# Optimization experiments

Measured on AMD Instinct MI355X. Metric: run time of the kernel, lower is better.

Reference implementation:

```python
import jax, jax.numpy as jnp
import numpy as np

N_PAPER = 200000
N_MESH = 30000
N = N_PAPER + N_MESH
D_PAPER = 512
D_MESH = 128
E_TRAIN = 2000000
E_POS = 500000
E_NEG = 500000


def setup_inputs() -> dict:
    key = jax.random.key(0)
    ks = jax.random.split(key, 32)

    def w(k, shape, fan_in):
        return jax.random.normal(k, shape, jnp.float32) / np.float32(np.sqrt(fan_in))

    inp = {}
    inp['x_paper'] = jax.random.normal(ks[0], (N_PAPER, D_PAPER), jnp.float32)
    inp['x_mesh'] = jax.random.normal(ks[1], (N_MESH, D_MESH), jnp.float32)
    # input transforms (stored as [in, out]; y = x @ W + b)
    inp['tp_w'] = w(ks[2], (D_PAPER, 16), D_PAPER)
    inp['tp_b'] = jnp.zeros((16,), jnp.float32)
    inp['tm_w'] = w(ks[3], (D_MESH, 16), D_MESH)
    inp['tm_b'] = jnp.zeros((16,), jnp.float32)
    # RGCN layers: basis decomposition W_r = sum_b comp[r,b] * basis[b]
    inp['comp1'] = w(ks[4], (2, 4), 4)
    inp['basis1'] = w(ks[5], (4, 16, 32), 16)
    inp['root1'] = w(ks[6], (16, 32), 16)
    inp['bias1'] = jnp.zeros((32,), jnp.float32)
    inp['comp2'] = w(ks[7], (2, 4), 4)
    inp['basis2'] = w(ks[8], (4, 32, 32), 32)
    inp['root2'] = w(ks[9], (32, 32), 32)
    inp['bias2'] = jnp.zeros((32,), jnp.float32)
    inp['comp3'] = w(ks[10], (2, 4), 4)
    inp['basis3'] = w(ks[11], (4, 32, 16), 32)
    inp['root3'] = w(ks[12], (32, 16), 32)
    inp['bias3'] = jnp.zeros((16,), jnp.float32)
    # decode linears (16 -> 16)
    inp['dpp_w'] = w(ks[13], (16, 16), 16)
    inp['dpp_b'] = jnp.zeros((16,), jnp.float32)
    inp['dpm_w'] = w(ks[14], (16, 16), 16)
    inp['dpm_b'] = jnp.zeros((16,), jnp.float32)
    # graph structure
    inp['train_edge_index'] = jax.random.randint(ks[15], (2, E_TRAIN), 0, N, jnp.int64)
    inp['train_edge_type'] = jax.random.randint(ks[16], (E_TRAIN,), 0, 2, jnp.int64)
    inp['pos_edge_index'] = jax.random.randint(ks[17], (2, E_POS), 0, N, jnp.int64)
    inp['pos_edge_type'] = jnp.sort(jax.random.randint(ks[18], (E_POS,), 0, 2, jnp.int64))
    inp['neg_edge_index'] = jax.random.randint(ks[19], (2, E_NEG), 0, N, jnp.int64)
    inp['neg_edge_type'] = jnp.sort(jax.random.randint(ks[20], (E_NEG,), 0, 2, jnp.int64))
    return inp


def rgcn(x, src, dst, etype, comp, basis, root, bias):
    # W: [R, in, out] from basis decomposition
    W = jnp.einsum('rb,bio->rio', comp, basis)
    # relation-typed message per edge (R == 2: compute both, select)
    xs = x[src]                                   # [E, in]  gather
    m = jnp.where((etype == 0)[:, None], xs @ W[0], xs @ W[1])  # [E, out]
    n = x.shape[0]
    agg = jax.ops.segment_sum(m, dst, num_segments=n)           # scatter-add
    deg = jax.ops.segment_sum(jnp.ones((src.shape[0],), x.dtype), dst, num_segments=n)
    agg = agg / jnp.maximum(deg, 1.0)[:, None]                   # mean aggregation
    return agg + x @ root + bias


def reference(x_paper, x_mesh, tp_w, tp_b, tm_w, tm_b,
              comp1, basis1, root1, bias1,
              comp2, basis2, root2, bias2,
              comp3, basis3, root3, bias3,
              dpp_w, dpp_b, dpm_w, dpm_b,
              train_edge_index, train_edge_type,
              pos_edge_index, pos_edge_type,
              neg_edge_index, neg_edge_type):
    # encode
    x = jnp.concatenate([x_paper @ tp_w + tp_b, x_mesh @ tm_w + tm_b], axis=0)
    src, dst = train_edge_index[0], train_edge_index[1]
    x = jax.nn.relu(rgcn(x, src, dst, train_edge_type, comp1, basis1, root1, bias1))
    x = jax.nn.relu(rgcn(x, src, dst, train_edge_type, comp2, basis2, root2, bias2))
    z = rgcn(x, src, dst, train_edge_type, comp3, basis3, root3, bias3)

    # decode: edge types are sorted, so per-edge type-select equals the
    # original mask-then-concat ordering [type0 ..., type1 ...]
    def edge_scores(ei, et):
        zs, zd = z[ei[0]], z[ei[1]]
        p = jnp.where((et == 0)[:, None], zs @ dpp_w + dpp_b, zs @ dpm_w + dpm_b)
        return (p * zd).sum(-1)

    return jnp.concatenate([edge_scores(pos_edge_index, pos_edge_type),
                            edge_scores(neg_edge_index, neg_edge_type)], axis=0)
```

## Files before the change

### kernel.cpp

```cpp
#include <hip/hip_runtime.h>

#define NPAPER 200000
#define NMESH  30000
#define NNODES 230000
#define ETRAIN 2000000
#define EPOS   500000
#define ENEG   500000

__device__ __forceinline__ void fma4(float4& a, float s, const float4 w) {
    a.x = fmaf(s, w.x, a.x);
    a.y = fmaf(s, w.y, a.y);
    a.z = fmaf(s, w.z, a.z);
    a.w = fmaf(s, w.w, a.w);
}

template <int D>
__global__ __launch_bounds__(256) void encode_kernel(
    const float* __restrict__ x, const float* __restrict__ w,
    const float* __restrict__ bias, float* __restrict__ out, int nrows) {
    __shared__ float wlds[D * 20];
    __shared__ float blds[16];
    for (int i = threadIdx.x; i < D * 16; i += 256)
        wlds[(i >> 4) * 20 + (i & 15)] = w[i];
    if (threadIdx.x < 16) blds[threadIdx.x] = bias[threadIdx.x];
    __syncthreads();

    const int lane = threadIdx.x & 63;
    const int row = blockIdx.x * 4 + (threadIdx.x >> 6);
    if (row >= nrows) return;

    const float* xr = x + (size_t)row * D;
    float4 acc[4];
#pragma unroll
    for (int g = 0; g < 4; g++) acc[g] = make_float4(0.f, 0.f, 0.f, 0.f);

#pragma unroll
    for (int t = 0; t < D / 64; t++) {
        const float xv = xr[t * 64 + lane];
        const float* wr = wlds + (t * 64 + lane) * 20;
#pragma unroll
        for (int g = 0; g < 4; g++)
            fma4(acc[g], xv, *reinterpret_cast<const float4*>(wr + 4 * g));
    }

#pragma unroll
    for (int g = 0; g < 4; g++) {
#pragma unroll
        for (int off = 32; off; off >>= 1) {
            acc[g].x += __shfl_xor(acc[g].x, off);
            acc[g].y += __shfl_xor(acc[g].y, off);
            acc[g].z += __shfl_xor(acc[g].z, off);
            acc[g].w += __shfl_xor(acc[g].w, off);
        }
    }
    if (lane == 0) {
        float4* orow = reinterpret_cast<float4*>(out + (size_t)row * 16);
#pragma unroll
        for (int g = 0; g < 4; g++) {
            const float4 b4 = *reinterpret_cast<const float4*>(blds + 4 * g);
            float4 o;
            o.x = acc[g].x + b4.x;
            o.y = acc[g].y + b4.y;
            o.z = acc[g].z + b4.z;
            o.w = acc[g].w + b4.w;
            orow[g] = o;
        }
    }
}

__global__ __launch_bounds__(256) void hist_kernel(const int* __restrict__ dst,
                                                   int* __restrict__ cnt) {
    const int e = blockIdx.x * 256 + threadIdx.x;
    if (e >= ETRAIN) return;
    atomicAdd(cnt + dst[e], 1);
}

__global__ __launch_bounds__(256) void scan1_kernel(const int* __restrict__ in,
                                                    int* __restrict__ out,
                                                    int* __restrict__ bsum,
                                                    int n) {
    __shared__ int s[256];
    const int tid = threadIdx.x;
    const int i = blockIdx.x * 256 + tid;
    const int v = (i < n) ? in[i] : 0;
    s[tid] = v;
    __syncthreads();
#pragma unroll
    for (int off = 1; off < 256; off <<= 1) {
        const int t = (tid >= off) ? s[tid - off] : 0;
        __syncthreads();
        s[tid] += t;
        __syncthreads();
    }
    if (i < n) out[i] = s[tid] - v;
    if (tid == 255) bsum[blockIdx.x] = s[255];
}

__global__ __launch_bounds__(256) void scan2_kernel(int* __restrict__ bsum,
                                                    int nb) {
    __shared__ int s[256];
    const int tid = threadIdx.x;
    int carry = 0;
    for (int base = 0; base < nb; base += 256) {
        const int i = base + tid;
        const int v = (i < nb) ? bsum[i] : 0;
        s[tid] = v;
        __syncthreads();
#pragma unroll
        for (int off = 1; off < 256; off <<= 1) {
            const int t = (tid >= off) ? s[tid - off] : 0;
            __syncthreads();
            s[tid] += t;
            __syncthreads();
        }
        if (i < nb) bsum[i] = s[tid] - v + carry;
        const int tot = s[255];
        __syncthreads();
        carry += tot;
    }
}

__global__ __launch_bounds__(256) void scan3_kernel(int* __restrict__ out,
                                                    const int* __restrict__ bsum,
                                                    int n) {
    const int i = blockIdx.x * 256 + threadIdx.x;
    if (i < n) out[i] += bsum[blockIdx.x];
}

__global__ __launch_bounds__(256) void fill_kernel(
    const int* __restrict__ src, const int* __restrict__ dst,
    const int* __restrict__ et, const int* __restrict__ rowptr,
    int* __restrict__ fc, int* __restrict__ esorted) {
    const int e = blockIdx.x * 256 + threadIdx.x;
    if (e >= ETRAIN) return;
    const int d = dst[e];
    const int pos = rowptr[d] + atomicAdd(fc + d, 1);
    esorted[pos] = src[e] | (et[e] << 24);
}

template <int IN, int OUT, bool RELU>
__global__ __launch_bounds__(256) void rgcn_gather_kernel(
    const float* __restrict__ x, const int* __restrict__ rowptr,
    const int* __restrict__ cnt, const int* __restrict__ esorted,
    const float* __restrict__ comp, const float* __restrict__ basis,
    const float* __restrict__ root, const float* __restrict__ bias,
    float* __restrict__ out) {
    constexpr int QP = OUT / 4;
    __shared__ float wlds[2 * IN * OUT];
    __shared__ float rlds[IN * OUT];
    __shared__ float blds[OUT];
    for (int i = threadIdx.x; i < 2 * IN * OUT; i += 256) {
        const int r = i / (IN * OUT);
        const int rem = i - r * IN * OUT;
        float v = 0.f;
#pragma unroll
        for (int b = 0; b < 4; b++)
            v = fmaf(comp[r * 4 + b], basis[b * IN * OUT + rem], v);
        wlds[i] = v;
    }
    for (int i = threadIdx.x; i < IN * OUT; i += 256) rlds[i] = root[i];
    if (threadIdx.x < OUT) blds[threadIdx.x] = bias[threadIdx.x];
    __syncthreads();

    const int gtid = blockIdx.x * 256 + threadIdx.x;
    const int n = gtid / QP;
    const int g = gtid % QP;
    if (n >= NNODES) return;

    const int begin = rowptr[n];
    const int c = cnt[n];

    float4 acc = make_float4(0.f, 0.f, 0.f, 0.f);
    for (int i = 0; i < c; i++) {
        const int pk = esorted[begin + i];
        const int s = pk & 0x00FFFFFF;
        const float* Wt = wlds + (pk >> 24) * (IN * OUT);
        const float4* xs = reinterpret_cast<const float4*>(x + (size_t)s * IN);
#pragma unroll
        for (int q = 0; q < IN / 4; q++) {
            const float4 xv = xs[q];
            const float* wq = Wt + (q * 4) * OUT + 4 * g;
            fma4(acc, xv.x, *reinterpret_cast<const float4*>(wq));
            fma4(acc, xv.y, *reinterpret_cast<const float4*>(wq + OUT));
            fma4(acc, xv.z, *reinterpret_cast<const float4*>(wq + 2 * OUT));
            fma4(acc, xv.w, *reinterpret_cast<const float4*>(wq + 3 * OUT));
        }
    }
    const float inv = 1.0f / fmaxf((float)c, 1.0f);
    float4 o = *reinterpret_cast<const float4*>(blds + 4 * g);
    o.x = fmaf(acc.x, inv, o.x);
    o.y = fmaf(acc.y, inv, o.y);
    o.z = fmaf(acc.z, inv, o.z);
    o.w = fmaf(acc.w, inv, o.w);

    const float4* xn = reinterpret_cast<const float4*>(x + (size_t)n * IN);
#pragma unroll
    for (int q = 0; q < IN / 4; q++) {
        const float4 xv = xn[q];
        const float* rq = rlds + (q * 4) * OUT + 4 * g;
        fma4(o, xv.x, *reinterpret_cast<const float4*>(rq));
        fma4(o, xv.y, *reinterpret_cast<const float4*>(rq + OUT));
        fma4(o, xv.z, *reinterpret_cast<const float4*>(rq + 2 * OUT));
        fma4(o, xv.w, *reinterpret_cast<const float4*>(rq + 3 * OUT));
    }
    if (RELU) {
        o.x = fmaxf(o.x, 0.f);
        o.y = fmaxf(o.y, 0.f);
        o.z = fmaxf(o.z, 0.f);
        o.w = fmaxf(o.w, 0.f);
    }
    reinterpret_cast<float4*>(out + (size_t)n * OUT)[g] = o;
}

__global__ __launch_bounds__(256) void decode_kernel(
    const float* __restrict__ z, const int* __restrict__ ei,
    const int* __restrict__ et, const float* __restrict__ wp,
    const float* __restrict__ bp, const float* __restrict__ wm,
    const float* __restrict__ bm, float* __restrict__ out, int E) {
    __shared__ float wl[2 * 256];
    __shared__ float bl[2 * 16];
    {
        const int i = threadIdx.x;
        wl[i] = wp[i];
        wl[256 + i] = wm[i];
        if (i < 16) {
            bl[i] = bp[i];
            bl[16 + i] = bm[i];
        }
    }
    __syncthreads();

    const int e = blockIdx.x * 256 + threadIdx.x;
    if (e >= E) return;
    const int s = ei[e], d = ei[e + E], t = et[e];

    const float4* zs4 = reinterpret_cast<const float4*>(z + (size_t)s * 16);
    const float4* zd4 = reinterpret_cast<const float4*>(z + (size_t)d * 16);
    float4 zs[4], zd[4];
#pragma unroll
    for (int q = 0; q < 4; q++) {
        zs[q] = zs4[q];
        zd[q] = zd4[q];
    }

    const float* W = wl + t * 256;
    const float* B = bl + t * 16;
    float4 p[4];
#pragma unroll
    for (int g = 0; g < 4; g++) p[g] = reinterpret_cast<const float4*>(B)[g];

#pragma unroll
    for (int q = 0; q < 4; q++) {
        const float xs[4] = {zs[q].x, zs[q].y, zs[q].z, zs[q].w};
#pragma unroll
        for (int c = 0; c < 4; c++) {
            const float4* wr =
                reinterpret_cast<const float4*>(W + (q * 4 + c) * 16);
#pragma unroll
            for (int g = 0; g < 4; g++) fma4(p[g], xs[c], wr[g]);
        }
    }
    float sc = 0.f;
#pragma unroll
    for (int g = 0; g < 4; g++) {
        sc += p[g].x * zd[g].x + p[g].y * zd[g].y + p[g].z * zd[g].z +
              p[g].w * zd[g].w;
    }
    out[e] = sc;
}

extern "C" void kernel_launch(void* const* d_in, const int* in_sizes, int n_in,
                              void* d_out, int out_size, void* d_ws,
                              size_t ws_size, hipStream_t stream) {
    const float* x_paper = (const float*)d_in[0];
    const float* x_mesh = (const float*)d_in[1];
    const float* tp_w = (const float*)d_in[2];
    const float* tp_b = (const float*)d_in[3];
    const float* tm_w = (const float*)d_in[4];
    const float* tm_b = (const float*)d_in[5];
    const float* comp1 = (const float*)d_in[6];
    const float* basis1 = (const float*)d_in[7];
    const float* root1 = (const float*)d_in[8];
    const float* bias1 = (const float*)d_in[9];
    const float* comp2 = (const float*)d_in[10];
    const float* basis2 = (const float*)d_in[11];
    const float* root2 = (const float*)d_in[12];
    const float* bias2 = (const float*)d_in[13];
    const float* comp3 = (const float*)d_in[14];
    const float* basis3 = (const float*)d_in[15];
    const float* root3 = (const float*)d_in[16];
    const float* bias3 = (const float*)d_in[17];
    const float* dpp_w = (const float*)d_in[18];
    const float* dpp_b = (const float*)d_in[19];
    const float* dpm_w = (const float*)d_in[20];
    const float* dpm_b = (const float*)d_in[21];
    const int* tei = (const int*)d_in[22];
    const int* tet = (const int*)d_in[23];
    const int* pei = (const int*)d_in[24];
    const int* pet = (const int*)d_in[25];
    const int* nei = (const int*)d_in[26];
    const int* net = (const int*)d_in[27];
    float* out = (float*)d_out;

    float* ws = (float*)d_ws;
    float* xfeat = ws;
    float* h1 = xfeat + (size_t)NNODES * 16;
    float* h2 = h1 + (size_t)NNODES * 32;
    int* rowptr = (int*)(h2 + (size_t)NNODES * 32);
    int* ecnt = rowptr + NNODES;
    int* fc = ecnt + NNODES;
    int* esorted = fc + NNODES;
    int* bsum = esorted + ETRAIN;
    float* z = xfeat;

    const int* tsrc = tei;
    const int* tdst = tei + ETRAIN;

    const int eblocks = (ETRAIN + 255) / 256;
    const int nb = (NNODES + 255) / 256;

    encode_kernel<512><<<(NPAPER + 3) / 4, 256, 0, stream>>>(
        x_paper, tp_w, tp_b, xfeat, NPAPER);
    encode_kernel<128><<<(NMESH + 3) / 4, 256, 0, stream>>>(
        x_mesh, tm_w, tm_b, xfeat + (size_t)NPAPER * 16, NMESH);

    hipMemsetAsync(ecnt, 0, (size_t)NNODES * 4, stream);
    hipMemsetAsync(fc, 0, (size_t)NNODES * 4, stream);
    hist_kernel<<<eblocks, 256, 0, stream>>>(tdst, ecnt);
    scan1_kernel<<<nb, 256, 0, stream>>>(ecnt, rowptr, bsum, NNODES);
    scan2_kernel<<<1, 256, 0, stream>>>(bsum, nb);
    scan3_kernel<<<nb, 256, 0, stream>>>(rowptr, bsum, NNODES);
    fill_kernel<<<eblocks, 256, 0, stream>>>(tsrc, tdst, tet, rowptr, fc,
                                             esorted);

    const int g32 = (NNODES * 8 + 255) / 256;
    const int g16 = (NNODES * 4 + 255) / 256;
    rgcn_gather_kernel<16, 32, true><<<g32, 256, 0, stream>>>(
        xfeat, rowptr, ecnt, esorted, comp1, basis1, root1, bias1, h1);
    rgcn_gather_kernel<32, 32, true><<<g32, 256, 0, stream>>>(
        h1, rowptr, ecnt, esorted, comp2, basis2, root2, bias2, h2);
    rgcn_gather_kernel<32, 16, false><<<g16, 256, 0, stream>>>(
        h2, rowptr, ecnt, esorted, comp3, basis3, root3, bias3, z);

    decode_kernel<<<(EPOS + 255) / 256, 256, 0, stream>>>(
        z, pei, pet, dpp_w, dpp_b, dpm_w, dpm_b, out, EPOS);
    decode_kernel<<<(ENEG + 255) / 256, 256, 0, stream>>>(
        z, nei, net, dpp_w, dpp_b, dpm_w, dpm_b, out + EPOS, ENEG);
}
```

Baseline: 1.365 ms.

## Aggregate neighbor features per relation before transform, and tile encode GEMM

The RGCN layers are split into an aggregation kernel and a combine kernel. The aggregation kernel has one thread per node, sums the mean-normalized source features separately for each relation, and prefetches the next edge index. The combine kernel then applies the relation weights and root weight once per node instead of once per edge, which removes the per-edge matrix multiply and the redundant gathers made by each output-quad thread. The encode kernel is retiled to stage 256 rows of x in LDS, with each thread computing 4 rows × 4 outputs instead of doing a wave-wide shuffle reduction per row. The cost is an extra intermediate buffer of 2*IN floats per node that must be written and read back, plus two more kernel launches per pair of layers.

New measurement: 1.238 ms. -9.3%, faster.

```diff
diff --git a/kernel.cpp b/kernel.cpp
--- a/kernel.cpp
+++ b/kernel.cpp
@@ -18,52 +18,68 @@
 __global__ __launch_bounds__(256) void encode_kernel(
     const float* __restrict__ x, const float* __restrict__ w,
     const float* __restrict__ bias, float* __restrict__ out, int nrows) {
-    __shared__ float wlds[D * 20];
+    constexpr int KP = 16;
+    __shared__ float wlds[D * 16];
+    __shared__ float xlds[256 * 20];
     __shared__ float blds[16];
-    for (int i = threadIdx.x; i < D * 16; i += 256)
-        wlds[(i >> 4) * 20 + (i & 15)] = w[i];
+
+    for (int i = threadIdx.x; i < D * 4; i += 256)
+        reinterpret_cast<float4*>(wlds)[i] =
+            reinterpret_cast<const float4*>(w)[i];
     if (threadIdx.x < 16) blds[threadIdx.x] = bias[threadIdx.x];
-    __syncthreads();
-
-    const int lane = threadIdx.x & 63;
-    const int row = blockIdx.x * 4 + (threadIdx.x >> 6);
-    if (row >= nrows) return;
-
-    const float* xr = x + (size_t)row * D;
+
+    const int g = threadIdx.x & 3;
+    const int rg = threadIdx.x >> 2;
+    const int row0 = blockIdx.x * 256;
+
     float4 acc[4];
 #pragma unroll
-    for (int g = 0; g < 4; g++) acc[g] = make_float4(0.f, 0.f, 0.f, 0.f);
-
-#pragma unroll
-    for (int t = 0; t < D / 64; t++) {
-        const float xv = xr[t * 64 + lane];
-        const float* wr = wlds + (t * 64 + lane) * 20;
-#pragma unroll
-        for (int g = 0; g < 4; g++)
-            fma4(acc[g], xv, *reinterpret_cast<const float4*>(wr + 4 * g));
-    }
-
-#pragma unroll
-    for (int g = 0; g < 4; g++) {
-#pragma unroll
-        for (int off = 32; off; off >>= 1) {
-            acc[g].x += __shfl_xor(acc[g].x, off);
-            acc[g].y += __shfl_xor(acc[g].y, off);
-            acc[g].z += __shfl_xor(acc[g].z, off);
-            acc[g].w += __shfl_xor(acc[g].w, off);
-        }
-    }
-    if (lane == 0) {
-        float4* orow = reinterpret_cast<float4*>(out + (size_t)row * 16);
-#pragma unroll
-        for (int g = 0; g < 4; g++) {
-            const float4 b4 = *reinterpret_cast<const float4*>(blds + 4 * g);
+    for (int j = 0; j < 4; j++) acc[j] = make_float4(0.f, 0.f, 0.f, 0.f);
+
+    for (int p = 0; p < D / KP; p++) {
+        __syncthreads();
+        for (int i = threadIdx.x; i < 1024; i += 256) {
+            const int rr = i >> 2, q = i & 3;
+            const int grow = min(row0 + rr, nrows - 1);
+            *reinterpret_cast<float4*>(xlds + rr * 20 + q * 4) =
+                *reinterpret_cast<const float4*>(x + (size_t)grow * D +
+                                                 p * KP + q * 4);
+        }
+        __syncthreads();
+#pragma unroll
+        for (int q = 0; q < KP / 4; q++) {
+            const int k = p * KP + q * 4;
+            const float4 w0 =
+                *reinterpret_cast<const float4*>(wlds + (k + 0) * 16 + 4 * g);
+            const float4 w1 =
+                *reinterpret_cast<const float4*>(wlds + (k + 1) * 16 + 4 * g);
+            const float4 w2 =
+                *reinterpret_cast<const float4*>(wlds + (k + 2) * 16 + 4 * g);
+            const float4 w3 =
+                *reinterpret_cast<const float4*>(wlds + (k + 3) * 16 + 4 * g);
+#pragma unroll
+            for (int j = 0; j < 4; j++) {
+                const float4 xv = *reinterpret_cast<const float4*>(
+                    xlds + (rg + 64 * j) * 20 + q * 4);
+                fma4(acc[j], xv.x, w0);
+                fma4(acc[j], xv.y, w1);
+                fma4(acc[j], xv.z, w2);
+                fma4(acc[j], xv.w, w3);
+            }
+        }
+    }
+
+    const float4 b4 = *reinterpret_cast<const float4*>(blds + 4 * g);
+#pragma unroll
+    for (int j = 0; j < 4; j++) {
+        const int grow = row0 + rg + 64 * j;
+        if (grow < nrows) {
             float4 o;
-            o.x = acc[g].x + b4.x;
-            o.y = acc[g].y + b4.y;
-            o.z = acc[g].z + b4.z;
-            o.w = acc[g].w + b4.w;
-            orow[g] = o;
+            o.x = acc[j].x + b4.x;
+            o.y = acc[j].y + b4.y;
+            o.z = acc[j].z + b4.z;
+            o.w = acc[j].w + b4.w;
+            *reinterpret_cast<float4*>(out + (size_t)grow * 16 + 4 * g) = o;
         }
     }
 }
@@ -138,28 +154,75 @@
     esorted[pos] = src[e] | (et[e] << 24);
 }
 
-template <int IN, int OUT, bool RELU>
-__global__ __launch_bounds__(256) void rgcn_gather_kernel(
+template <int IN>
+__global__ __launch_bounds__(256) void agg_kernel(
     const float* __restrict__ x, const int* __restrict__ rowptr,
     const int* __restrict__ cnt, const int* __restrict__ esorted,
+    float* __restrict__ sx) {
+    const int n = blockIdx.x * 256 + threadIdx.x;
+    if (n >= NNODES) return;
+    const int b = rowptr[n], c = cnt[n];
+
+    float4 s0[IN / 4], s1[IN / 4];
+#pragma unroll
+    for (int q = 0; q < IN / 4; q++) {
+        s0[q] = make_float4(0.f, 0.f, 0.f, 0.f);
+        s1[q] = make_float4(0.f, 0.f, 0.f, 0.f);
+    }
+
+    int pk = (c > 0) ? esorted[b] : 0;
+    for (int i = 0; i < c; i++) {
+        const int pknext = (i + 1 < c) ? esorted[b + i + 1] : 0;
+        const int s = pk & 0x00FFFFFF;
+        const float w1 = (float)(pk >> 24);
+        const float w0 = 1.0f - w1;
+        const float4* xs =
+            reinterpret_cast<const float4*>(x + (size_t)s * IN);
+#pragma unroll
+        for (int q = 0; q < IN / 4; q++) {
+            const float4 xv = xs[q];
+            fma4(s0[q], w0, xv);
+            fma4(s1[q], w1, xv);
+        }
+        pk = pknext;
+    }
+    const float inv = 1.0f / fmaxf((float)c, 1.0f);
+    float4* o = reinterpret_cast<float4*>(sx + (size_t)n * (2 * IN));
+#pragma unroll
+    for (int q = 0; q < IN / 4; q++) {
+        float4 v = s0[q];
+        v.x *= inv; v.y *= inv; v.z *= inv; v.w *= inv;
+        o[q] = v;
+    }
+#pragma unroll
+    for (int q = 0; q < IN / 4; q++) {
+        float4 v = s1[q];
+        v.x *= inv; v.y *= inv; v.z *= inv; v.w *= inv;
+        o[IN / 4 + q] = v;
+    }
+}
+
+template <int IN, int OUT, bool RELU>
+__global__ __launch_bounds__(256) void combine2_kernel(
+    const float* __restrict__ xin, const float* __restrict__ sx,
     const float* __restrict__ comp, const float* __restrict__ basis,
     const float* __restrict__ root, const float* __restrict__ bias,
     float* __restrict__ out) {
     constexpr int QP = OUT / 4;
-    __shared__ float wlds[2 * IN * OUT];
-    __shared__ float rlds[IN * OUT];
-    __shared__ float blds[OUT];
+    __shared__ float wl[3 * IN * OUT];
+    __shared__ float bl[OUT];
     for (int i = threadIdx.x; i < 2 * IN * OUT; i += 256) {
         const int r = i / (IN * OUT);
         const int rem = i - r * IN * OUT;
         float v = 0.f;
 #pragma unroll
-        for (int b = 0; b < 4; b++)
-            v = fmaf(comp[r * 4 + b], basis[b * IN * OUT + rem], v);
-        wlds[i] = v;
-    }
-    for (int i = threadIdx.x; i < IN * OUT; i += 256) rlds[i] = root[i];
-    if (threadIdx.x < OUT) blds[threadIdx.x] = bias[threadIdx.x];
+        for (int bb = 0; bb < 4; bb++)
+            v = fmaf(comp[r * 4 + bb], basis[bb * IN * OUT + rem], v);
+        wl[i] = v;
+    }
+    for (int i = threadIdx.x; i < IN * OUT; i += 256)
+        wl[2 * IN * OUT + i] = root[i];
+    if (threadIdx.x < OUT) bl[threadIdx.x] = bias[threadIdx.x];
     __syncthreads();
 
     const int gtid = blockIdx.x * 256 + threadIdx.x;
@@ -167,49 +230,37 @@
     const int g = gtid % QP;
     if (n >= NNODES) return;
 
-    const int begin = rowptr[n];
-    const int c = cnt[n];
-
-    float4 acc = make_float4(0.f, 0.f, 0.f, 0.f);
-    for (int i = 0; i < c; i++) {
-        const int pk = esorted[begin + i];
-        const int s = pk & 0x00FFFFFF;
-        const float* Wt = wlds + (pk >> 24) * (IN * OUT);
-        const float4* xs = reinterpret_cast<const float4*>(x + (size_t)s * IN);
-#pragma unroll
-        for (int q = 0; q < IN / 4; q++) {
-            const float4 xv = xs[q];
-            const float* wq = Wt + (q * 4) * OUT + 4 * g;
-            fma4(acc, xv.x, *reinterpret_cast<const float4*>(wq));
-            fma4(acc, xv.y, *reinterpret_cast<const float4*>(wq + OUT));
-            fma4(acc, xv.z, *reinterpret_cast<const float4*>(wq + 2 * OUT));
-            fma4(acc, xv.w, *reinterpret_cast<const float4*>(wq + 3 * OUT));
-        }
-    }
-    const float inv = 1.0f / fmaxf((float)c, 1.0f);
-    float4 o = *reinterpret_cast<const float4*>(blds + 4 * g);
-    o.x = fmaf(acc.x, inv, o.x);
-    o.y = fmaf(acc.y, inv, o.y);
-    o.z = fmaf(acc.z, inv, o.z);
-    o.w = fmaf(acc.w, inv, o.w);
-
-    const float4* xn = reinterpret_cast<const float4*>(x + (size_t)n * IN);
+    float4 acc = *reinterpret_cast<const float4*>(bl + 4 * g);
+
+    const float4* iv1 =
+        reinterpret_cast<const float4*>(sx + (size_t)n * (2 * IN));
+#pragma unroll
+    for (int q = 0; q < 2 * IN / 4; q++) {
+        const float4 xv = iv1[q];
+        const float* wr = wl + (q * 4) * OUT + 4 * g;
+        fma4(acc, xv.x, *reinterpret_cast<const float4*>(wr));
+        fma4(acc, xv.y, *reinterpret_cast<const float4*>(wr + OUT));
+        fma4(acc, xv.z, *reinterpret_cast<const float4*>(wr + 2 * OUT));
+        fma4(acc, xv.w, *reinterpret_cast<const float4*>(wr + 3 * OUT));
+    }
+    const float4* iv2 =
+        reinterpret_cast<const float4*>(xin + (size_t)n * IN);
 #pragma unroll
     for (int q = 0; q < IN / 4; q++) {
-        const float4 xv = xn[q];
-        const float* rq = rlds + (q * 4) * OUT + 4 * g;
-        fma4(o, xv.x, *reinterpret_cast<const float4*>(rq));
-        fma4(o, xv.y, *reinterpret_cast<const float4*>(rq + OUT));
-        fma4(o, xv.z, *reinterpret_cast<const float4*>(rq + 2 * OUT));
-        fma4(o, xv.w, *reinterpret_cast<const float4*>(rq + 3 * OUT));
+        const float4 xv = iv2[q];
+        const float* wr = wl + (2 * IN + q * 4) * OUT + 4 * g;
+        fma4(acc, xv.x, *reinterpret_cast<const float4*>(wr));
+        fma4(acc, xv.y, *reinterpret_cast<const float4*>(wr + OUT));
+        fma4(acc, xv.z, *reinterpret_cast<const float4*>(wr + 2 * OUT));
+        fma4(acc, xv.w, *reinterpret_cast<const float4*>(wr + 3 * OUT));
     }
     if (RELU) {
-        o.x = fmaxf(o.x, 0.f);
-        o.y = fmaxf(o.y, 0.f);
-        o.z = fmaxf(o.z, 0.f);
-        o.w = fmaxf(o.w, 0.f);
-    }
-    reinterpret_cast<float4*>(out + (size_t)n * OUT)[g] = o;
+        acc.x = fmaxf(acc.x, 0.f);
+        acc.y = fmaxf(acc.y, 0.f);
+        acc.z = fmaxf(acc.z, 0.f);
+        acc.w = fmaxf(acc.w, 0.f);
+    }
+    reinterpret_cast<float4*>(out + (size_t)n * OUT)[g] = acc;
 }
 
 __global__ __launch_bounds__(256) void decode_kernel(
@@ -303,15 +354,20 @@
     float* out = (float*)d_out;
 
     float* ws = (float*)d_ws;
-    float* xfeat = ws;
-    float* h1 = xfeat + (size_t)NNODES * 16;
-    float* h2 = h1 + (size_t)NNODES * 32;
-    int* rowptr = (int*)(h2 + (size_t)NNODES * 32);
+    float* R1 = ws;
+    float* R2 = R1 + (size_t)NNODES * 32;
+    float* R3 = R2 + (size_t)NNODES * 32;
+    float* xfeat = R2;
+    float* h1 = R1;
+    float* h2 = R2;
+    float* sx = R3;
+    float* z = R1;
+
+    int* rowptr = (int*)(R3 + (size_t)NNODES * 64);
     int* ecnt = rowptr + NNODES;
     int* fc = ecnt + NNODES;
     int* esorted = fc + NNODES;
     int* bsum = esorted + ETRAIN;
-    float* z = xfeat;
 
     const int* tsrc = tei;
     const int* tdst = tei + ETRAIN;
@@ -319,9 +375,9 @@
     const int eblocks = (ETRAIN + 255) / 256;
     const int nb = (NNODES + 255) / 256;
 
-    encode_kernel<512><<<(NPAPER + 3) / 4, 256, 0, stream>>>(
+    encode_kernel<512><<<(NPAPER + 255) / 256, 256, 0, stream>>>(
         x_paper, tp_w, tp_b, xfeat, NPAPER);
-    encode_kernel<128><<<(NMESH + 3) / 4, 256, 0, stream>>>(
+    encode_kernel<128><<<(NMESH + 255) / 256, 256, 0, stream>>>(
         x_mesh, tm_w, tm_b, xfeat + (size_t)NPAPER * 16, NMESH);
 
     hipMemsetAsync(ecnt, 0, (size_t)NNODES * 4, stream);
@@ -333,14 +389,19 @@
     fill_kernel<<<eblocks, 256, 0, stream>>>(tsrc, tdst, tet, rowptr, fc,
                                              esorted);
 
-    const int g32 = (NNODES * 8 + 255) / 256;
-    const int g16 = (NNODES * 4 + 255) / 256;
-    rgcn_gather_kernel<16, 32, true><<<g32, 256, 0, stream>>>(
-        xfeat, rowptr, ecnt, esorted, comp1, basis1, root1, bias1, h1);
-    rgcn_gather_kernel<32, 32, true><<<g32, 256, 0, stream>>>(
-        h1, rowptr, ecnt, esorted, comp2, basis2, root2, bias2, h2);
-    rgcn_gather_kernel<32, 16, false><<<g16, 256, 0, stream>>>(
-        h2, rowptr, ecnt, esorted, comp3, basis3, root3, bias3, z);
+    agg_kernel<16><<<nb, 256, 0, stream>>>(xfeat, rowptr, ecnt, esorted, sx);
+    combine2_kernel<16, 32, true>
+        <<<(NNODES * 8 + 255) / 256, 256, 0, stream>>>(xfeat, sx, comp1,
+                                                       basis1, root1, bias1,
+                                                       h1);
+    agg_kernel<32><<<nb, 256, 0, stream>>>(h1, rowptr, ecnt, esorted, sx);
+    combine2_kernel<32, 32, true>
+        <<<(NNODES * 8 + 255) / 256, 256, 0, stream>>>(h1, sx, comp2, basis2,
+                                                       root2, bias2, h2);
+    agg_kernel<32><<<nb, 256, 0, stream>>>(h2, rowptr, ecnt, esorted, sx);
+    combine2_kernel<32, 16, false>
+        <<<(NNODES * 4 + 255) / 256, 256, 0, stream>>>(h2, sx, comp3, basis3,
+                                                       root3, bias3, z);
 
     decode_kernel<<<(EPOS + 255) / 256, 256, 0, stream>>>(
         z, pei, pet, dpp_w, dpp_b, dpm_w, dpm_b, out, EPOS);
```
